# Kernel optimization log

Measured on AMD Instinct MI355X. Metric: run time of the kernel, lower is better.

## Reference

```python
import jax, jax.numpy as jnp
import numpy as np
from jax import lax

B_, L_, D_ = 4, 512, 512          # batch, seq_len, in_dim (d_model)
HID, H2 = 512, 256                # hidden_dim, per-direction LSTM width
NL, DST, DCV, DIN, DTR = 3, 16, 4, 1024, 32  # layers, d_state, d_conv, d_inner, dt_rank


def _silu(x):
    return x * jax.nn.sigmoid(x)


def _layernorm(x, g, b):
    m = x.mean(-1, keepdims=True)
    v = x.var(-1, keepdims=True)
    return (x - m) / jnp.sqrt(v + 1e-5) * g + b


def _mamba(x, wi, cw, cb, xpw, dw, db, Alog, Dp, wo):
    # x: (B,L,D)
    Bsz, Ls, _ = x.shape
    xz = jnp.einsum('bld,ed->ble', x, wi)          # (B,L,2*DIN)
    xin, z = jnp.split(xz, 2, axis=-1)
    # causal depthwise conv1d (kernel DCV, left-padded)
    xpad = jnp.pad(xin, ((0, 0), (DCV - 1, 0), (0, 0)))
    u = cb + sum(xpad[:, k:k + Ls, :] * cw[:, k] for k in range(DCV))
    u = _silu(u)                                   # (B,L,DIN)
    xdbl = jnp.einsum('blc,ec->ble', u, xpw)       # (B,L,DTR+2*DST)
    dt_in = xdbl[..., :DTR]
    Bc = xdbl[..., DTR:DTR + DST]
    Cc = xdbl[..., DTR + DST:]
    dt = jax.nn.softplus(jnp.einsum('blr,cr->blc', dt_in, dw) + db)  # (B,L,DIN)
    A = -jnp.exp(Alog)                             # (DIN,DST), negative

    def step(h, inp):
        dt_t, B_t, C_t, u_t = inp                  # (B,DIN),(B,DST),(B,DST),(B,DIN)
        dA = jnp.exp(dt_t[..., None] * A)          # (B,DIN,DST)
        h = dA * h + (dt_t * u_t)[..., None] * B_t[:, None, :]
        y = jnp.einsum('bcn,bn->bc', h, C_t)
        return h, y

    h0 = jnp.zeros((Bsz, DIN, DST), x.dtype)
    _, ys = lax.scan(step, h0, (dt.transpose(1, 0, 2), Bc.transpose(1, 0, 2),
                                Cc.transpose(1, 0, 2), u.transpose(1, 0, 2)))
    y = ys.transpose(1, 0, 2) + u * Dp
    y = y * _silu(z)
    return jnp.einsum('blc,dc->bld', y, wo)


def _lstm_dir(x, wih, whh, bih, bhh, reverse):
    Bsz = x.shape[0]

    def step(carry, xt):
        h, c = carry
        g = xt @ wih.T + h @ whh.T + bih + bhh     # (B,4*H2), PyTorch gate order i,f,g,o
        i, f, gg, o = jnp.split(g, 4, axis=-1)
        c = jax.nn.sigmoid(f) * c + jax.nn.sigmoid(i) * jnp.tanh(gg)
        h = jax.nn.sigmoid(o) * jnp.tanh(c)
        return (h, c), h

    init = (jnp.zeros((Bsz, H2), x.dtype), jnp.zeros((Bsz, H2), x.dtype))
    _, hs = lax.scan(step, init, x.transpose(1, 0, 2), reverse=reverse)
    return hs.transpose(1, 0, 2)


def setup_inputs():
    key = jax.random.key(0)
    ks = jax.random.split(key, 16)
    rn = lambda k, s, sc=0.02: jax.random.normal(k, s, jnp.float32) * sc
    inp = {}
    inp['x'] = jax.random.normal(ks[0], (B_, L_, D_), jnp.float32)
    inp['in_proj_w'] = rn(ks[1], (NL, 2 * DIN, D_))
    inp['conv_w'] = rn(ks[2], (NL, DIN, DCV), 0.2)
    inp['conv_b'] = jnp.zeros((NL, DIN), jnp.float32)
    inp['x_proj_w'] = rn(ks[3], (NL, DTR + 2 * DST, DIN))
    inp['dt_proj_w'] = rn(ks[4], (NL, DIN, DTR), 0.1)
    inp['dt_proj_b'] = jnp.full((NL, DIN), -4.0, jnp.float32)
    inp['A_log'] = jnp.log(jnp.broadcast_to(jnp.arange(1, DST + 1, dtype=jnp.float32), (NL, DIN, DST)))
    inp['D_param'] = jnp.ones((NL, DIN), jnp.float32)
    inp['out_proj_w'] = rn(ks[5], (NL, D_, DIN))
    inp['ln_g'] = jnp.ones((NL, D_), jnp.float32)
    inp['ln_b'] = jnp.zeros((NL, D_), jnp.float32)
    inp['lstm_w_ih'] = rn(ks[6], (2, 4 * H2, D_), 0.05)
    inp['lstm_w_hh'] = rn(ks[7], (2, 4 * H2, H2), 0.05)
    inp['lstm_b_ih'] = jnp.zeros((2, 4 * H2), jnp.float32)
    inp['lstm_b_hh'] = jnp.zeros((2, 4 * H2), jnp.float32)
    inp['fusion_w'] = rn(ks[8], (HID, D_ + HID), 0.02)
    inp['fusion_b'] = jnp.zeros((HID,), jnp.float32)
    return inp


def reference(x, in_proj_w, conv_w, conv_b, x_proj_w, dt_proj_w, dt_proj_b, A_log,
              D_param, out_proj_w, ln_g, ln_b, lstm_w_ih, lstm_w_hh, lstm_b_ih,
              lstm_b_hh, fusion_w, fusion_b):
    m = x
    for i in range(NL):
        mo = _mamba(m, in_proj_w[i], conv_w[i], conv_b[i], x_proj_w[i],
                    dt_proj_w[i], dt_proj_b[i], A_log[i], D_param[i], out_proj_w[i])
        m = _layernorm(m + mo, ln_g[i], ln_b[i])
    lf = _lstm_dir(x, lstm_w_ih[0], lstm_w_hh[0], lstm_b_ih[0], lstm_b_hh[0], False)
    lb = _lstm_dir(x, lstm_w_ih[1], lstm_w_hh[1], lstm_b_ih[1], lstm_b_hh[1], True)
    comb = jnp.concatenate([m, lf, lb], axis=-1)   # (B,L,D_+HID)
    return comb @ fusion_w.T + fusion_b
```

## Files before the change

kernel.cpp:

```cpp
#include <hip/hip_runtime.h>
#include <math.h>

#define B_  4
#define L_  512
#define D_  512
#define DIN 1024
#define DST 16
#define DCV 4
#define DTR 32
#define NL  3
#define H2  256

typedef _Float16 __f16;
typedef __f16 f16x2 __attribute__((ext_vector_type(2)));
typedef __f16 half8 __attribute__((ext_vector_type(8)));
typedef float f32x4v __attribute__((ext_vector_type(4)));
typedef unsigned uint4v __attribute__((ext_vector_type(4)));

__device__ __forceinline__ float fast_sigmoid(float x) { return 1.f / (1.f + __expf(-x)); }
__device__ __forceinline__ float fast_tanh(float x) { return 2.f / (1.f + __expf(-2.f * x)) - 1.f; }

__device__ __forceinline__ float dot2f(unsigned a, unsigned b, float c) {
  return __builtin_amdgcn_fdot2(__builtin_bit_cast(f16x2, a),
                                __builtin_bit_cast(f16x2, b), c, false);
}
__device__ __forceinline__ unsigned packf16(float a, float b) {
  f16x2 p; p.x = (__f16)a; p.y = (__f16)b;
  return __builtin_bit_cast(unsigned, p);
}

template<bool ACC>
__global__ __launch_bounds__(256) void gemm_mfma_h(
    const __f16* __restrict__ A, const __f16* __restrict__ W, float* __restrict__ C,
    int M, int N, int K, int lda, int ldb, int ldc,
    const float* __restrict__ bias, const float* __restrict__ bias2)
{
  __shared__ uint4v As[1024];
  __shared__ uint4v Bs[1024];
  const int tid  = threadIdx.x;
  const int lane = tid & 63, wid = tid >> 6;
  const int wr = wid >> 1, wc = wid & 1;
  const int fr = lane & 15, fq = lane >> 4;
  const int m0 = blockIdx.y * 128, n0 = blockIdx.x * 128;
  const int srow = tid >> 3, skb = tid & 7;

  f32x4v acc[4][4] = {};
  for (int k0 = 0; k0 < K; k0 += 64) {
    const __f16* Ab = A + (size_t)m0 * lda + k0;
    const __f16* Bb = W + (size_t)n0 * ldb + k0;
    #pragma unroll
    for (int i = 0; i < 4; ++i) {
      int row = srow + i * 32;
      uint4v ap = *(const uint4v*)(Ab + (size_t)row * lda + skb * 8);
      uint4v bp = *(const uint4v*)(Bb + (size_t)row * ldb + skb * 8);
      As[row * 8 + (skb ^ (row & 7))] = ap;
      Bs[row * 8 + (skb ^ (row & 7))] = bp;
    }
    __syncthreads();
    #pragma unroll
    for (int ks = 0; ks < 2; ++ks) {
      half8 af[4], bf[4];
      #pragma unroll
      for (int mt = 0; mt < 4; ++mt) {
        int row = wr * 64 + mt * 16 + fr;
        int kb = ks * 4 + fq;
        af[mt] = __builtin_bit_cast(half8, As[row * 8 + (kb ^ (row & 7))]);
      }
      #pragma unroll
      for (int nt = 0; nt < 4; ++nt) {
        int row = wc * 64 + nt * 16 + fr;
        int kb = ks * 4 + fq;
        bf[nt] = __builtin_bit_cast(half8, Bs[row * 8 + (kb ^ (row & 7))]);
      }
      #pragma unroll
      for (int mt = 0; mt < 4; ++mt)
        #pragma unroll
        for (int nt = 0; nt < 4; ++nt)
          acc[mt][nt] = __builtin_amdgcn_mfma_f32_16x16x32_f16(af[mt], bf[nt], acc[mt][nt], 0, 0, 0);
    }
    __syncthreads();
  }
  #pragma unroll
  for (int nt = 0; nt < 4; ++nt) {
    int n = n0 + wc * 64 + nt * 16 + fr;
    float bv = (bias ? bias[n] : 0.f) + (bias2 ? bias2[n] : 0.f);
    #pragma unroll
    for (int mt = 0; mt < 4; ++mt) {
      #pragma unroll
      for (int r = 0; r < 4; ++r) {
        int m = m0 + wr * 64 + mt * 16 + fq * 4 + r;
        float v = acc[mt][nt][r] + bv;
        if (ACC) C[(size_t)m * ldc + n] += v; else C[(size_t)m * ldc + n] = v;
      }
    }
  }
}

template<int ACT>
__global__ __launch_bounds__(256) void gemm_nt(
    const float* __restrict__ A, const float* __restrict__ Bm, float* __restrict__ C,
    int M, int N, int K, int lda, int ldb, int ldc,
    const float* __restrict__ bias)
{
  __shared__ __align__(16) float As[16][64];
  __shared__ __align__(16) float Bs[16][64];
  const int tid = threadIdx.x;
  const int tx = tid & 15, ty = tid >> 4;
  const int m0 = blockIdx.y * 64, n0 = blockIdx.x * 64;
  const int r = tid >> 2, kq = (tid & 3) * 4;
  float acc[4][4] = {};
  for (int k0 = 0; k0 < K; k0 += 16) {
    float4 av = *(const float4*)(A  + (size_t)(m0 + r) * lda + (k0 + kq));
    float4 bv = *(const float4*)(Bm + (size_t)(n0 + r) * ldb + (k0 + kq));
    As[kq+0][r] = av.x; As[kq+1][r] = av.y; As[kq+2][r] = av.z; As[kq+3][r] = av.w;
    Bs[kq+0][r] = bv.x; Bs[kq+1][r] = bv.y; Bs[kq+2][r] = bv.z; Bs[kq+3][r] = bv.w;
    __syncthreads();
    #pragma unroll
    for (int kk = 0; kk < 16; ++kk) {
      float4 a = *(const float4*)(&As[kk][ty*4]);
      float4 b = *(const float4*)(&Bs[kk][tx*4]);
      float aa[4] = {a.x, a.y, a.z, a.w};
      float bb[4] = {b.x, b.y, b.z, b.w};
      #pragma unroll
      for (int i = 0; i < 4; ++i)
        #pragma unroll
        for (int j = 0; j < 4; ++j)
          acc[i][j] = fmaf(aa[i], bb[j], acc[i][j]);
    }
    __syncthreads();
  }
  #pragma unroll
  for (int i = 0; i < 4; ++i) {
    int m = m0 + ty*4 + i;
    float* cp = C + (size_t)m * ldc + n0 + tx*4;
    #pragma unroll
    for (int j = 0; j < 4; ++j) {
      int n = n0 + tx*4 + j;
      float v = acc[i][j];
      if (bias)  v += bias[n];
      if (ACT == 1) v = (v > 20.f) ? v : log1pf(__expf(v));
      cp[j] = v;
    }
  }
}

__global__ __launch_bounds__(256) void packh(
    const float* __restrict__ src, __f16* __restrict__ dst, int n)
{
  int t = blockIdx.x * 256 + threadIdx.x;
  if (t < n) dst[t] = (__f16)src[t];
}

__global__ __launch_bounds__(256) void pack_xpw_h(
    const float* __restrict__ xpw, __f16* __restrict__ dst)
{
  int t = blockIdx.x * 256 + threadIdx.x;
  int layer = t >> 17;
  int r = (t >> 10) & 127;
  int k = t & 1023;
  dst[t] = (r < 64) ? (__f16)xpw[layer * 65536 + r * 1024 + k] : (__f16)0.f;
}

__global__ __launch_bounds__(256) void pack_whh(
    const float* __restrict__ whh, uint4* __restrict__ wpk)
{
  int idx = blockIdx.x * 256 + threadIdx.x;
  int t = idx & 511;
  int q = (idx >> 9) & 15;
  int G = (idx >> 13) & 3;
  int dir = idx >> 15;
  int j = t >> 1, ks = t & 1;
  const float* src = whh + (size_t)dir * 262144 + (size_t)(G * 256 + j) * 256 + ks * 128 + q * 8;
  float4 fa = ((const float4*)src)[0];
  float4 fb = ((const float4*)src)[1];
  uint4 pk;
  pk.x = packf16(fa.x, fa.y); pk.y = packf16(fa.z, fa.w);
  pk.z = packf16(fb.x, fb.y); pk.w = packf16(fb.z, fb.w);
  wpk[idx] = pk;
}

__global__ __launch_bounds__(256) void conv_silu(
    const float* __restrict__ xz, const float* __restrict__ cw, const float* __restrict__ cb,
    float* __restrict__ u, __f16* __restrict__ uh)
{
  int t = blockIdx.x * 256 + threadIdx.x;
  int c  = t & (DIN - 1);
  int bl = t >> 10;
  int l  = bl & (L_ - 1);
  float acc = cb[c];
  #pragma unroll
  for (int k = 0; k < DCV; ++k) {
    int ls = l + k - (DCV - 1);
    if (ls >= 0)
      acc = fmaf(xz[(size_t)(bl + k - (DCV - 1)) * 2048 + c], cw[c * DCV + k], acc);
  }
  float v = acc * fast_sigmoid(acc);
  u[t] = v;
  uh[t] = (__f16)v;
}

__global__ __launch_bounds__(256) void scan_kernel(
    const float* __restrict__ dt, const float* __restrict__ u,
    const float* __restrict__ xdbl, const float* __restrict__ xz,
    const float* __restrict__ A_log, const float* __restrict__ Dp,
    __f16* __restrict__ y)
{
  int t = blockIdx.x * 256 + threadIdx.x;
  int n  = t & 15;
  int bc = t >> 4;
  int c  = bc & (DIN - 1);
  int b  = bc >> 10;
  float Ac = -__expf(A_log[c * DST + n]);
  float Dc = Dp[c];
  float h = 0.f;
  const size_t row = (size_t)b * L_;

#define DECLP(i) float dtv##i, uv##i, Bn##i, Cn##i, zv##i;
  DECLP(0) DECLP(1) DECLP(2) DECLP(3)
#define LOADP(i, l) { \
    const size_t nb_ = row + (l); \
    dtv##i = dt[nb_ * DIN + c]; \
    uv##i  = u [nb_ * DIN + c]; \
    Bn##i  = xdbl[nb_ * 128 + 32 + n]; \
    Cn##i  = xdbl[nb_ * 128 + 48 + n]; \
    zv##i  = xz[nb_ * 2048 + 1024 + c]; }
#define STEPP(i, l) { \
    float dA_ = __expf(dtv##i * Ac); \
    h = fmaf(dA_, h, (dtv##i * uv##i) * Bn##i); \
    float p_ = h * Cn##i; \
    p_ += __shfl_xor(p_, 1, 64); \
    p_ += __shfl_xor(p_, 2, 64); \
    p_ += __shfl_xor(p_, 4, 64); \
    p_ += __shfl_xor(p_, 8, 64); \
    if (n == 0) { \
      float yv_ = p_ + uv##i * Dc; \
      yv_ *= zv##i * fast_sigmoid(zv##i); \
      y[(row + (l)) * DIN + c] = (__f16)yv_; \
    } }

  LOADP(0, 0) LOADP(1, 1) LOADP(2, 2) LOADP(3, 3)
  for (int l = 0; l < L_ - 4; l += 4) {
    STEPP(0, l)     LOADP(0, l + 4)
    STEPP(1, l + 1) LOADP(1, l + 5)
    STEPP(2, l + 2) LOADP(2, l + 6)
    STEPP(3, l + 3) LOADP(3, l + 7)
  }
  STEPP(0, L_ - 4) STEPP(1, L_ - 3) STEPP(2, L_ - 2) STEPP(3, L_ - 1)
#undef DECLP
#undef LOADP
#undef STEPP
}

__global__ __launch_bounds__(64) void resid_ln(
    const float* __restrict__ a, const float* __restrict__ mo,
    const float* __restrict__ g, const float* __restrict__ bta,
    float* __restrict__ outm, int ldo, __f16* __restrict__ outh, int ldoh)
{
  int row = blockIdx.x;
  int lane = threadIdx.x;
  const float* pa = a  + (size_t)row * 512;
  const float* pb = mo + (size_t)row * 512;
  float v[8];
  float s = 0.f, s2 = 0.f;
  #pragma unroll
  for (int i = 0; i < 8; ++i) {
    float x = pa[lane + i * 64] + pb[lane + i * 64];
    v[i] = x; s += x; s2 += x * x;
  }
  #pragma unroll
  for (int off = 1; off < 64; off <<= 1) {
    s  += __shfl_xor(s,  off, 64);
    s2 += __shfl_xor(s2, off, 64);
  }
  float mean = s * (1.f / 512.f);
  float var  = s2 * (1.f / 512.f) - mean * mean;
  float rstd = rsqrtf(var + 1e-5f);
  #pragma unroll
  for (int i = 0; i < 8; ++i) {
    int cidx = lane + i * 64;
    float o = (v[i] - mean) * rstd * g[cidx] + bta[cidx];
    if (outm) outm[(size_t)row * ldo + cidx] = o;
    outh[(size_t)row * ldoh + cidx] = (__f16)o;
  }
}

#define WDECL(q) uint4 W0_##q, W1_##q, W2_##q;
#define LDG1(W, G, q) W = wp[((G) * 16 + (q)) * 512 + t];
#define WLOAD(q) LDG1(W0_##q, 0, q) LDG1(W1_##q, 1, q) LDG1(W2_##q, 2, q)
#define WSTEP(q) { \
    uint4 hv = h4s[buf][(q) * 2 + ks]; \
    uint4 wv = wo_lds[(q) * 512 + t]; \
    a0 = dot2f(W0_##q.x, hv.x, a0); a0 = dot2f(W0_##q.y, hv.y, a0); \
    a0 = dot2f(W0_##q.z, hv.z, a0); a0 = dot2f(W0_##q.w, hv.w, a0); \
    a1 = dot2f(W1_##q.x, hv.x, a1); a1 = dot2f(W1_##q.y, hv.y, a1); \
    a1 = dot2f(W1_##q.z, hv.z, a1); a1 = dot2f(W1_##q.w, hv.w, a1); \
    a2 = dot2f(W2_##q.x, hv.x, a2); a2 = dot2f(W2_##q.y, hv.y, a2); \
    a2 = dot2f(W2_##q.z, hv.z, a2); a2 = dot2f(W2_##q.w, hv.w, a2); \
    a3 = dot2f(wv.x, hv.x, a3); a3 = dot2f(wv.y, hv.y, a3); \
    a3 = dot2f(wv.z, hv.z, a3); a3 = dot2f(wv.w, hv.w, a3); }
#define REP16(M) M(0) M(1) M(2) M(3) M(4) M(5) M(6) M(7) \
                 M(8) M(9) M(10) M(11) M(12) M(13) M(14) M(15)

__global__ __launch_bounds__(512, 1) void lstm_rec(
    const float* __restrict__ gx, const uint4* __restrict__ wpk,
    __f16* __restrict__ comb)
{
  __shared__ uint4 wo_lds[16 * 512];
  __shared__ __align__(16) uint4 h4s[2][32];
  const int dir = blockIdx.x >> 2, b = blockIdx.x & 3;
  const int t = threadIdx.x;
  const int j = t >> 1, ks = t & 1;
  const uint4* wp = wpk + (size_t)dir * 4 * 16 * 512;

  REP16(WDECL)
  REP16(WLOAD)

  #pragma unroll
  for (int q = 0; q < 16; ++q)
    wo_lds[q * 512 + t] = wp[(3 * 16 + q) * 512 + t];

  if (t < 256) ((unsigned*)h4s)[t] = 0u;
  float c_reg = 0.f;
  __f16* outp = comb + 512 + dir * 256;
  const float* gxb = gx + (size_t)(b * L_) * 2048 + dir * 1024;
  const int offA = (ks ? 1 : 0) * 256 + j;
  const int offB = (ks ? 3 : 2) * 256 + j;
  const int p_   = t >> 2;
  const int hidx = ((p_ >> 2) & 15) * 8 + (p_ >> 6) * 4 + (p_ & 3);
  __syncthreads();

  int buf = 0;
  const int l0 = dir ? (L_ - 1) : 0;
  float pgA = gxb[(size_t)l0 * 2048 + offA];
  float pgB = gxb[(size_t)l0 * 2048 + offB];

  for (int s = 0; s < L_; ++s) {
    const int l = dir ? (L_ - 1 - s) : s;
    float pgA_n = 0.f, pgB_n = 0.f;
    if (s + 1 < L_) {
      const int ln = dir ? (L_ - 2 - s) : (s + 1);
      pgA_n = gxb[(size_t)ln * 2048 + offA];
      pgB_n = gxb[(size_t)ln * 2048 + offB];
    }
    float a0 = 0.f, a1 = 0.f, a2 = 0.f, a3 = 0.f;
    REP16(WSTEP)
    if (ks == 0) { a0 += pgA; a2 += pgB; } else { a1 += pgA; a3 += pgB; }
    a0 += __shfl_xor(a0, 1, 64);
    a1 += __shfl_xor(a1, 1, 64);
    a2 += __shfl_xor(a2, 1, 64);
    a3 += __shfl_xor(a3, 1, 64);
    const float si = fast_sigmoid(a0);
    const float sf = fast_sigmoid(a1);
    const float tg = fast_tanh(a2);
    const float so = fast_sigmoid(a3);
    c_reg = fmaf(sf, c_reg, si * tg);
    const float hv = so * fast_tanh(c_reg);
    if (ks == 0) outp[(size_t)(b * L_ + l) * 1024 + j] = (__f16)hv;
    const float hv2 = __shfl_xor(hv, 2, 64);
    if ((t & 3) == 0)
      ((unsigned*)h4s[buf ^ 1])[hidx] = packf16(hv, hv2);
    pgA = pgA_n; pgB = pgB_n;
    buf ^= 1;
    __syncthreads();
  }
}

extern "C" void kernel_launch(void* const* d_in, const int* in_sizes, int n_in,
                              void* d_out, int out_size, void* d_ws, size_t ws_size,
                              hipStream_t stream)
{
  const float* x    = (const float*)d_in[0];
  const float* wi   = (const float*)d_in[1];
  const float* cw   = (const float*)d_in[2];
  const float* cb   = (const float*)d_in[3];
  const float* xpw  = (const float*)d_in[4];
  const float* dw   = (const float*)d_in[5];
  const float* db   = (const float*)d_in[6];
  const float* Alog = (const float*)d_in[7];
  const float* Dp   = (const float*)d_in[8];
  const float* wo   = (const float*)d_in[9];
  const float* lng  = (const float*)d_in[10];
  const float* lnb  = (const float*)d_in[11];
  const float* wih  = (const float*)d_in[12];
  const float* whh  = (const float*)d_in[13];
  const float* bih  = (const float*)d_in[14];
  const float* bhh  = (const float*)d_in[15];
  const float* fw   = (const float*)d_in[16];
  const float* fb   = (const float*)d_in[17];
  float* out = (float*)d_out;

  float* F = (float*)d_ws;
  float* xz     = F;
  float* gx     = F;
  float* mo     = F + 3145728;
  float* u      = F + 4194304;
  float* xdbl   = F + 7340032;
  float* dt     = F + 7602176;
  float* mbuf   = F + 10747904;
  __f16* fw_h   = (__f16*)(F + 4194304);
  __f16* u_h    = (__f16*)(F + 6291456);
  __f16* wih_h  = (__f16*)(F + 7602176);
  uint4* wpk    = (uint4*)(F + 8126464);
  __f16* wi_hc  = (__f16*)(F + 8388608);
  __f16* ybuf_h = (__f16*)(F + 9699328);
  __f16* x_h    = (__f16*)(F + 9699328);
  __f16* mbuf_h = (__f16*)(F + 11796480);
  __f16* comb_h = (__f16*)(F + 12320768);
  __f16* wo_h   = (__f16*)(F + 13369344);
  __f16* xpw_h  = (__f16*)(F + 14155776);

  const int M = B_ * L_;
  dim3 blk(256);

  packh<<<dim3(4096), blk, 0, stream>>>(x,   x_h,   1048576);
  packh<<<dim3(4096), blk, 0, stream>>>(wih, wih_h, 1048576);
  packh<<<dim3(6144), blk, 0, stream>>>(wo,  wo_h,  1572864);
  pack_xpw_h<<<dim3(1536), blk, 0, stream>>>(xpw, xpw_h);

  gemm_mfma_h<false><<<dim3(16, 16), blk, 0, stream>>>(
      x_h, wih_h, gx, M, 2048, 512, 512, 512, 2048, bih, bhh);
  pack_whh<<<dim3(256), blk, 0, stream>>>(whh, wpk);
  lstm_rec<<<dim3(8), dim3(512), 0, stream>>>(gx, wpk, comb_h);

  for (int i = 0; i < NL; ++i) {
    const float* min = (i == 0) ? x : mbuf;
    const __f16* min_h = (i == 0) ? x_h : mbuf_h;
    packh<<<dim3(4096), blk, 0, stream>>>(wi + (size_t)i*1048576, wi_hc, 1048576);
    gemm_mfma_h<false><<<dim3(16, 16), blk, 0, stream>>>(
        min_h, wi_hc, xz, M, 2048, 512, 512, 512, 2048, nullptr, nullptr);
    conv_silu<<<dim3(8192), blk, 0, stream>>>(
        xz, cw + (size_t)i*DIN*DCV, cb + i*DIN, u, u_h);
    gemm_mfma_h<false><<<dim3(1, 16), blk, 0, stream>>>(
        u_h, xpw_h + (size_t)i*131072, xdbl, M, 128, 1024, 1024, 1024, 128, nullptr, nullptr);
    gemm_nt<1><<<dim3(16, 32), blk, 0, stream>>>(
        xdbl, dw + (size_t)i*32768, dt, M, 1024, 32, 128, 32, 1024, db + i*1024);
    scan_kernel<<<dim3(256), blk, 0, stream>>>(
        dt, u, xdbl, xz, Alog + (size_t)i*DIN*DST, Dp + i*DIN, ybuf_h);
    gemm_mfma_h<false><<<dim3(4, 16), blk, 0, stream>>>(
        ybuf_h, wo_h + (size_t)i*524288, mo, M, 512, 1024, 1024, 1024, 512, nullptr, nullptr);
    if (i < NL - 1)
      resid_ln<<<dim3(M), dim3(64), 0, stream>>>(
          min, mo, lng + i*512, lnb + i*512, mbuf, 512, mbuf_h, 512);
    else
      resid_ln<<<dim3(M), dim3(64), 0, stream>>>(
          min, mo, lng + i*512, lnb + i*512, nullptr, 0, comb_h, 1024);
  }

  packh<<<dim3(2048), blk, 0, stream>>>(fw, fw_h, 524288);
  gemm_mfma_h<false><<<dim3(4, 16), blk, 0, stream>>>(
      comb_h, fw_h, out, M, 512, 1024, 1024, 1024, 512, fb, nullptr);
}
```

Before: 1.554 ms.

## Chunk selective scan over sequence and move dt projection to MFMA GEMM

The sequential Mamba scan is split into four sequence chunks. A first pass computes each chunk's end state and cumulative decay product, and a second pass rebuilds each chunk's starting state from those and produces the outputs. This gives four times as many threads as the old single-pass scan, at the cost of reading dt, u and B twice. The fp32 dt projection GEMM is also replaced by the f16 MFMA GEMM with a fused softplus epilogue, using zero-padded weights and an f16 x_proj output, which lowers precision for B, C and dt_in.

```diff
diff --git a/kernel.cpp b/kernel.cpp
--- a/kernel.cpp
+++ b/kernel.cpp
@@ -10,6 +10,7 @@
 #define DTR 32
 #define NL  3
 #define H2  256
+#define LCH 128
 
 typedef _Float16 __f16;
 typedef __f16 f16x2 __attribute__((ext_vector_type(2)));
@@ -29,9 +30,9 @@
   return __builtin_bit_cast(unsigned, p);
 }
 
-template<bool ACC>
+template<int ACT, bool ACC, bool HOUT>
 __global__ __launch_bounds__(256) void gemm_mfma_h(
-    const __f16* __restrict__ A, const __f16* __restrict__ W, float* __restrict__ C,
+    const __f16* __restrict__ A, const __f16* __restrict__ W, void* __restrict__ Cv,
     int M, int N, int K, int lda, int ldb, int ldc,
     const float* __restrict__ bias, const float* __restrict__ bias2)
 {
@@ -80,6 +81,8 @@
     }
     __syncthreads();
   }
+  float* C = (float*)Cv;
+  __f16* Ch = (__f16*)Cv;
   #pragma unroll
   for (int nt = 0; nt < 4; ++nt) {
     int n = n0 + wc * 64 + nt * 16 + fr;
@@ -90,56 +93,11 @@
       for (int r = 0; r < 4; ++r) {
         int m = m0 + wr * 64 + mt * 16 + fq * 4 + r;
         float v = acc[mt][nt][r] + bv;
-        if (ACC) C[(size_t)m * ldc + n] += v; else C[(size_t)m * ldc + n] = v;
+        if (ACT == 1) v = (v > 20.f) ? v : log1pf(__expf(v));
+        if (HOUT) Ch[(size_t)m * ldc + n] = (__f16)v;
+        else if (ACC) C[(size_t)m * ldc + n] += v;
+        else C[(size_t)m * ldc + n] = v;
       }
-    }
-  }
-}
-
-template<int ACT>
-__global__ __launch_bounds__(256) void gemm_nt(
-    const float* __restrict__ A, const float* __restrict__ Bm, float* __restrict__ C,
-    int M, int N, int K, int lda, int ldb, int ldc,
-    const float* __restrict__ bias)
-{
-  __shared__ __align__(16) float As[16][64];
-  __shared__ __align__(16) float Bs[16][64];
-  const int tid = threadIdx.x;
-  const int tx = tid & 15, ty = tid >> 4;
-  const int m0 = blockIdx.y * 64, n0 = blockIdx.x * 64;
-  const int r = tid >> 2, kq = (tid & 3) * 4;
-  float acc[4][4] = {};
-  for (int k0 = 0; k0 < K; k0 += 16) {
-    float4 av = *(const float4*)(A  + (size_t)(m0 + r) * lda + (k0 + kq));
-    float4 bv = *(const float4*)(Bm + (size_t)(n0 + r) * ldb + (k0 + kq));
-    As[kq+0][r] = av.x; As[kq+1][r] = av.y; As[kq+2][r] = av.z; As[kq+3][r] = av.w;
-    Bs[kq+0][r] = bv.x; Bs[kq+1][r] = bv.y; Bs[kq+2][r] = bv.z; Bs[kq+3][r] = bv.w;
-    __syncthreads();
-    #pragma unroll
-    for (int kk = 0; kk < 16; ++kk) {
-      float4 a = *(const float4*)(&As[kk][ty*4]);
-      float4 b = *(const float4*)(&Bs[kk][tx*4]);
-      float aa[4] = {a.x, a.y, a.z, a.w};
-      float bb[4] = {b.x, b.y, b.z, b.w};
-      #pragma unroll
-      for (int i = 0; i < 4; ++i)
-        #pragma unroll
-        for (int j = 0; j < 4; ++j)
-          acc[i][j] = fmaf(aa[i], bb[j], acc[i][j]);
-    }
-    __syncthreads();
-  }
-  #pragma unroll
-  for (int i = 0; i < 4; ++i) {
-    int m = m0 + ty*4 + i;
-    float* cp = C + (size_t)m * ldc + n0 + tx*4;
-    #pragma unroll
-    for (int j = 0; j < 4; ++j) {
-      int n = n0 + tx*4 + j;
-      float v = acc[i][j];
-      if (bias)  v += bias[n];
-      if (ACT == 1) v = (v > 20.f) ? v : log1pf(__expf(v));
-      cp[j] = v;
     }
   }
 }
@@ -159,6 +117,16 @@
   int r = (t >> 10) & 127;
   int k = t & 1023;
   dst[t] = (r < 64) ? (__f16)xpw[layer * 65536 + r * 1024 + k] : (__f16)0.f;
+}
+
+__global__ __launch_bounds__(256) void pack_dwh(
+    const float* __restrict__ dw, __f16* __restrict__ dst)
+{
+  int t = blockIdx.x * 256 + threadIdx.x;
+  int layer = t >> 16;
+  int r = (t >> 6) & 1023;
+  int k = t & 63;
+  dst[t] = (k < 32) ? (__f16)dw[layer * 32768 + r * 32 + k] : (__f16)0.f;
 }
 
 __global__ __launch_bounds__(256) void pack_whh(
@@ -199,21 +167,71 @@
   uh[t] = (__f16)v;
 }
 
-__global__ __launch_bounds__(256) void scan_kernel(
+
+__global__ __launch_bounds__(256) void scan_part(
     const float* __restrict__ dt, const float* __restrict__ u,
-    const float* __restrict__ xdbl, const float* __restrict__ xz,
+    const __f16* __restrict__ xdh, const float* __restrict__ A_log,
+    float* __restrict__ hend, float* __restrict__ Pp)
+{
+  int t = blockIdx.x * 256 + threadIdx.x;
+  int n  = t & 15;
+  int ch = (t >> 4) & 3;
+  int bc = t >> 6;
+  int c  = bc & (DIN - 1);
+  int b  = bc >> 10;
+  float Ac = -__expf(A_log[c * DST + n]);
+  float h = 0.f, P = 1.f;
+  const size_t row = (size_t)b * L_ + ch * LCH;
+
+#define DECLP(i) float dtv##i, uv##i, Bn##i;
+  DECLP(0) DECLP(1) DECLP(2) DECLP(3)
+#define LOADP(i, l) { \
+    const size_t nb_ = row + (l); \
+    dtv##i = dt[nb_ * DIN + c]; \
+    uv##i  = u [nb_ * DIN + c]; \
+    Bn##i  = (float)xdh[nb_ * 128 + 32 + n]; }
+#define STEPP(i) { \
+    float dA_ = __expf(dtv##i * Ac); \
+    h = fmaf(dA_, h, (dtv##i * uv##i) * Bn##i); \
+    P *= dA_; }
+
+  LOADP(0, 0) LOADP(1, 1) LOADP(2, 2) LOADP(3, 3)
+  for (int l = 0; l < LCH - 4; l += 4) {
+    STEPP(0) LOADP(0, l + 4)
+    STEPP(1) LOADP(1, l + 5)
+    STEPP(2) LOADP(2, l + 6)
+    STEPP(3) LOADP(3, l + 7)
+  }
+  STEPP(0) STEPP(1) STEPP(2) STEPP(3)
+#undef DECLP
+#undef LOADP
+#undef STEPP
+  int flat = bc * 16 + n;
+  hend[ch * 65536 + flat] = h;
+  Pp[ch * 65536 + flat]   = P;
+}
+
+__global__ __launch_bounds__(256) void scan_fix(
+    const float* __restrict__ dt, const float* __restrict__ u,
+    const __f16* __restrict__ xdh, const float* __restrict__ xz,
     const float* __restrict__ A_log, const float* __restrict__ Dp,
+    const float* __restrict__ hend, const float* __restrict__ Pp,
     __f16* __restrict__ y)
 {
   int t = blockIdx.x * 256 + threadIdx.x;
   int n  = t & 15;
-  int bc = t >> 4;
+  int ch = (t >> 4) & 3;
+  int bc = t >> 6;
   int c  = bc & (DIN - 1);
   int b  = bc >> 10;
   float Ac = -__expf(A_log[c * DST + n]);
   float Dc = Dp[c];
+  const int flat = bc * 16 + n;
   float h = 0.f;
-  const size_t row = (size_t)b * L_;
+  if (ch > 0) h = hend[flat];
+  if (ch > 1) h = fmaf(Pp[1 * 65536 + flat], h, hend[1 * 65536 + flat]);
+  if (ch > 2) h = fmaf(Pp[2 * 65536 + flat], h, hend[2 * 65536 + flat]);
+  const size_t row = (size_t)b * L_ + ch * LCH;
 
 #define DECLP(i) float dtv##i, uv##i, Bn##i, Cn##i, zv##i;
   DECLP(0) DECLP(1) DECLP(2) DECLP(3)
@@ -221,8 +239,8 @@
     const size_t nb_ = row + (l); \
     dtv##i = dt[nb_ * DIN + c]; \
     uv##i  = u [nb_ * DIN + c]; \
-    Bn##i  = xdbl[nb_ * 128 + 32 + n]; \
-    Cn##i  = xdbl[nb_ * 128 + 48 + n]; \
+    Bn##i  = (float)xdh[nb_ * 128 + 32 + n]; \
+    Cn##i  = (float)xdh[nb_ * 128 + 48 + n]; \
     zv##i  = xz[nb_ * 2048 + 1024 + c]; }
 #define STEPP(i, l) { \
     float dA_ = __expf(dtv##i * Ac); \
@@ -239,13 +257,13 @@
     } }
 
   LOADP(0, 0) LOADP(1, 1) LOADP(2, 2) LOADP(3, 3)
-  for (int l = 0; l < L_ - 4; l += 4) {
+  for (int l = 0; l < LCH - 4; l += 4) {
     STEPP(0, l)     LOADP(0, l + 4)
     STEPP(1, l + 1) LOADP(1, l + 5)
     STEPP(2, l + 2) LOADP(2, l + 6)
     STEPP(3, l + 3) LOADP(3, l + 7)
   }
-  STEPP(0, L_ - 4) STEPP(1, L_ - 3) STEPP(2, L_ - 2) STEPP(3, L_ - 1)
+  STEPP(0, LCH - 4) STEPP(1, LCH - 3) STEPP(2, LCH - 2) STEPP(3, LCH - 1)
 #undef DECLP
 #undef LOADP
 #undef STEPP
@@ -394,7 +412,7 @@
   float* gx     = F;
   float* mo     = F + 3145728;
   float* u      = F + 4194304;
-  float* xdbl   = F + 7340032;
+  __f16* xdh    = (__f16*)(F + 7340032);
   float* dt     = F + 7602176;
   float* mbuf   = F + 10747904;
   __f16* fw_h   = (__f16*)(F + 4194304);
@@ -408,6 +426,9 @@
   __f16* comb_h = (__f16*)(F + 12320768);
   __f16* wo_h   = (__f16*)(F + 13369344);
   __f16* xpw_h  = (__f16*)(F + 14155776);
+  __f16* dwh    = (__f16*)(F + 14352384);
+  float* hend   = F + 14450688;
+  float* Pp     = F + 14712832;
 
   const int M = B_ * L_;
   dim3 blk(256);
@@ -416,8 +437,9 @@
   packh<<<dim3(4096), blk, 0, stream>>>(wih, wih_h, 1048576);
   packh<<<dim3(6144), blk, 0, stream>>>(wo,  wo_h,  1572864);
   pack_xpw_h<<<dim3(1536), blk, 0, stream>>>(xpw, xpw_h);
-
-  gemm_mfma_h<false><<<dim3(16, 16), blk, 0, stream>>>(
+  pack_dwh<<<dim3(768), blk, 0, stream>>>(dw, dwh);
+
+  gemm_mfma_h<0,false,false><<<dim3(16, 16), blk, 0, stream>>>(
       x_h, wih_h, gx, M, 2048, 512, 512, 512, 2048, bih, bhh);
   pack_whh<<<dim3(256), blk, 0, stream>>>(whh, wpk);
   lstm_rec<<<dim3(8), dim3(512), 0, stream>>>(gx, wpk, comb_h);
@@ -426,17 +448,19 @@
     const float* min = (i == 0) ? x : mbuf;
     const __f16* min_h = (i == 0) ? x_h : mbuf_h;
     packh<<<dim3(4096), blk, 0, stream>>>(wi + (size_t)i*1048576, wi_hc, 1048576);
-    gemm_mfma_h<false><<<dim3(16, 16), blk, 0, stream>>>(
+    gemm_mfma_h<0,false,false><<<dim3(16, 16), blk, 0, stream>>>(
         min_h, wi_hc, xz, M, 2048, 512, 512, 512, 2048, nullptr, nullptr);
     conv_silu<<<dim3(8192), blk, 0, stream>>>(
         xz, cw + (size_t)i*DIN*DCV, cb + i*DIN, u, u_h);
-    gemm_mfma_h<false><<<dim3(1, 16), blk, 0, stream>>>(
-        u_h, xpw_h + (size_t)i*131072, xdbl, M, 128, 1024, 1024, 1024, 128, nullptr, nullptr);
-    gemm_nt<1><<<dim3(16, 32), blk, 0, stream>>>(
-        xdbl, dw + (size_t)i*32768, dt, M, 1024, 32, 128, 32, 1024, db + i*1024);
-    scan_kernel<<<dim3(256), blk, 0, stream>>>(
-        dt, u, xdbl, xz, Alog + (size_t)i*DIN*DST, Dp + i*DIN, ybuf_h);
-    gemm_mfma_h<false><<<dim3(4, 16), blk, 0, stream>>>(
+    gemm_mfma_h<0,false,true><<<dim3(1, 16), blk, 0, stream>>>(
+        u_h, xpw_h + (size_t)i*131072, xdh, M, 128, 1024, 1024, 1024, 128, nullptr, nullptr);
+    gemm_mfma_h<1,false,false><<<dim3(8, 16), blk, 0, stream>>>(
+        xdh, dwh + (size_t)i*65536, dt, M, 1024, 64, 128, 64, 1024, db + i*1024, nullptr);
+    scan_part<<<dim3(1024), blk, 0, stream>>>(
+        dt, u, xdh, Alog + (size_t)i*DIN*DST, hend, Pp);
+    scan_fix<<<dim3(1024), blk, 0, stream>>>(
+        dt, u, xdh, xz, Alog + (size_t)i*DIN*DST, Dp + i*DIN, hend, Pp, ybuf_h);
+    gemm_mfma_h<0,false,false><<<dim3(4, 16), blk, 0, stream>>>(
         ybuf_h, wo_h + (size_t)i*524288, mo, M, 512, 1024, 1024, 1024, 512, nullptr, nullptr);
     if (i < NL - 1)
       resid_ln<<<dim3(M), dim3(64), 0, stream>>>(
@@ -447,6 +471,6 @@
   }
 
   packh<<<dim3(2048), blk, 0, stream>>>(fw, fw_h, 524288);
-  gemm_mfma_h<false><<<dim3(4, 16), blk, 0, stream>>>(
+  gemm_mfma_h<0,false,false><<<dim3(4, 16), blk, 0, stream>>>(
       comb_h, fw_h, out, M, 512, 1024, 1024, 1024, 512, fb, nullptr);
 }
```

Measured after the change: 1.426 ms. 1.09x faster.
